# Kernel optimization log

Measured on AMD Instinct MI355X. Metric: run time of the kernel, lower is better.

## Reference

```python
import jax, jax.numpy as jnp
import numpy as np

B, L, V, D = 2048, 128, 30522, 768


def setup_inputs() -> dict:
    key = jax.random.key(0)
    k_len, k_ids, k_emb = jax.random.split(key, 3)
    # left-contiguous attention mask (HF convention), lengths in [1, L]
    lengths = jax.random.randint(k_len, (B,), 1, L + 1)
    tag_attention_mask = (jnp.arange(L)[None, :] < lengths[:, None]).astype(jnp.int32)
    tag_input_ids = jax.random.randint(k_ids, (B, L), 0, V).astype(jnp.int64)
    emb_weight = jax.random.normal(k_emb, (V, D), dtype=jnp.float32) * 0.02
    return {
        "tag_input_ids": tag_input_ids,
        "tag_attention_mask": tag_attention_mask,
        "emb_weight": emb_weight,
    }


def reference(tag_input_ids, tag_attention_mask, emb_weight):
    # embedding lookup: [B, L, D]
    tag_text_embeds = emb_weight[tag_input_ids]
    # masked mean pooling over the ragged valid prefix. Equivalent to the
    # original per-sample slice+mean loop because the mask is left-contiguous.
    m = (tag_attention_mask == 1).astype(tag_text_embeds.dtype)  # [B, L]
    summed = jnp.einsum("bld,bl->bd", tag_text_embeds, m)        # [B, D]
    counts = jnp.sum(m, axis=-1, keepdims=True)                   # [B, 1]
    return summed / counts
```

## Files before the change

### kernel.cpp

```cpp
#include <hip/hip_runtime.h>

#define BB 2048
#define LL 128
#define DD 768
#define NT 192
#define DV (DD / 4)

__global__ __launch_bounds__(NT) void masked_mean_pool_kernel(
    const int* __restrict__ ids,
    const int* __restrict__ mask,
    const float* __restrict__ emb,
    float* __restrict__ out)
{
    const int b = blockIdx.x;
    const int t = threadIdx.x;

    __shared__ int s_ids[LL];
    __shared__ int s_part[2];

    if (t < LL) {
        s_ids[t] = ids[b * LL + t];
        int m = mask[b * LL + t];
        unsigned long long bal = __ballot(m != 0);
        if ((t & 63) == 0) s_part[t >> 6] = __popcll(bal);
    }
    __syncthreads();

    const int cnt = s_part[0] + s_part[1];

    const float4* __restrict__ embv = reinterpret_cast<const float4*>(emb);

    float ax = 0.f, ay = 0.f, az = 0.f, aw = 0.f;

    int l = 0;
    for (; l + 8 <= cnt; l += 8) {
        float4 r0 = embv[s_ids[l + 0] * DV + t];
        float4 r1 = embv[s_ids[l + 1] * DV + t];
        float4 r2 = embv[s_ids[l + 2] * DV + t];
        float4 r3 = embv[s_ids[l + 3] * DV + t];
        float4 r4 = embv[s_ids[l + 4] * DV + t];
        float4 r5 = embv[s_ids[l + 5] * DV + t];
        float4 r6 = embv[s_ids[l + 6] * DV + t];
        float4 r7 = embv[s_ids[l + 7] * DV + t];
        ax += r0.x + r1.x + r2.x + r3.x + r4.x + r5.x + r6.x + r7.x;
        ay += r0.y + r1.y + r2.y + r3.y + r4.y + r5.y + r6.y + r7.y;
        az += r0.z + r1.z + r2.z + r3.z + r4.z + r5.z + r6.z + r7.z;
        aw += r0.w + r1.w + r2.w + r3.w + r4.w + r5.w + r6.w + r7.w;
    }
    for (; l < cnt; ++l) {
        float4 r = embv[s_ids[l] * DV + t];
        ax += r.x; ay += r.y; az += r.z; aw += r.w;
    }

    const float inv = 1.0f / (float)cnt;
    float4 o;
    o.x = ax * inv; o.y = ay * inv; o.z = az * inv; o.w = aw * inv;
    reinterpret_cast<float4*>(out)[b * DV + t] = o;
}

extern "C" void kernel_launch(void* const* d_in, const int* in_sizes, int n_in,
                              void* d_out, int out_size, void* d_ws, size_t ws_size,
                              hipStream_t stream) {
    const int*   ids  = (const int*)d_in[0];
    const int*   mask = (const int*)d_in[1];
    const float* emb  = (const float*)d_in[2];
    float*       out  = (float*)d_out;

    masked_mean_pool_kernel<<<BB, NT, 0, stream>>>(ids, mask, emb, out);
}
```

Baseline: 64.81 us.

## Split sequence into chunks across blocks with two-pass partial-sum reduction

Splits each batch row's sequence into four 32-token chunks, each handled by its own block that writes a partial sum to workspace. A second kernel adds the valid partials and divides by the count. The aim is to balance load across ragged lengths and raise the number of blocks for better latency hiding, at the cost of a second launch and extra workspace traffic. The old single-kernel path is kept as a fallback when the workspace is too small.

Result: slower. 83.20 us (+28.4%).

```diff
diff --git a/kernel.cpp b/kernel.cpp
--- a/kernel.cpp
+++ b/kernel.cpp
@@ -5,6 +5,93 @@
 #define DD 768
 #define NT 192
 #define DV (DD / 4)
+#define CHUNK 32
+#define CH (LL / CHUNK)
+
+__global__ __launch_bounds__(NT) void partial_sum_kernel(
+    const int* __restrict__ ids,
+    const int* __restrict__ mask,
+    const float* __restrict__ emb,
+    float* __restrict__ ws)
+{
+    const int bc = blockIdx.x;
+    const int b  = bc >> 2;
+    const int c  = bc & 3;
+    const int t  = threadIdx.x;
+
+    __shared__ int s_ids[CHUNK];
+    __shared__ int s_part[2];
+
+    if (t < LL) {
+        int m = mask[b * LL + t];
+        unsigned long long bal = __ballot(m != 0);
+        if ((t & 63) == 0) s_part[t >> 6] = __popcll(bal);
+    }
+    __syncthreads();
+    const int cnt = s_part[0] + s_part[1];
+
+    const int l0 = c * CHUNK;
+    const int n  = min(cnt, l0 + CHUNK) - l0;
+    if (n <= 0) return;
+
+    if (t < n) s_ids[t] = ids[b * LL + l0 + t];
+    __syncthreads();
+
+    const float4* __restrict__ embv = reinterpret_cast<const float4*>(emb);
+
+    float ax = 0.f, ay = 0.f, az = 0.f, aw = 0.f;
+    int l = 0;
+    for (; l + 8 <= n; l += 8) {
+        float4 r0 = embv[s_ids[l + 0] * DV + t];
+        float4 r1 = embv[s_ids[l + 1] * DV + t];
+        float4 r2 = embv[s_ids[l + 2] * DV + t];
+        float4 r3 = embv[s_ids[l + 3] * DV + t];
+        float4 r4 = embv[s_ids[l + 4] * DV + t];
+        float4 r5 = embv[s_ids[l + 5] * DV + t];
+        float4 r6 = embv[s_ids[l + 6] * DV + t];
+        float4 r7 = embv[s_ids[l + 7] * DV + t];
+        ax += r0.x + r1.x + r2.x + r3.x + r4.x + r5.x + r6.x + r7.x;
+        ay += r0.y + r1.y + r2.y + r3.y + r4.y + r5.y + r6.y + r7.y;
+        az += r0.z + r1.z + r2.z + r3.z + r4.z + r5.z + r6.z + r7.z;
+        aw += r0.w + r1.w + r2.w + r3.w + r4.w + r5.w + r6.w + r7.w;
+    }
+    for (; l < n; ++l) {
+        float4 r = embv[s_ids[l] * DV + t];
+        ax += r.x; ay += r.y; az += r.z; aw += r.w;
+    }
+
+    float4 o; o.x = ax; o.y = ay; o.z = az; o.w = aw;
+    reinterpret_cast<float4*>(ws)[bc * DV + t] = o;
+}
+
+__global__ __launch_bounds__(NT) void finalize_kernel(
+    const int* __restrict__ mask,
+    const float* __restrict__ ws,
+    float* __restrict__ out)
+{
+    const int b = blockIdx.x;
+    const int t = threadIdx.x;
+
+    __shared__ int s_part[2];
+    if (t < LL) {
+        int m = mask[b * LL + t];
+        unsigned long long bal = __ballot(m != 0);
+        if ((t & 63) == 0) s_part[t >> 6] = __popcll(bal);
+    }
+    __syncthreads();
+    const int cnt = s_part[0] + s_part[1];
+    const int nch = (cnt + CHUNK - 1) >> 5;
+
+    const float4* __restrict__ wsv = reinterpret_cast<const float4*>(ws);
+    float4 a = wsv[(b * CH + 0) * DV + t];
+    for (int c = 1; c < nch; ++c) {
+        float4 p = wsv[(b * CH + c) * DV + t];
+        a.x += p.x; a.y += p.y; a.z += p.z; a.w += p.w;
+    }
+    const float inv = 1.0f / (float)cnt;
+    a.x *= inv; a.y *= inv; a.z *= inv; a.w *= inv;
+    reinterpret_cast<float4*>(out)[b * DV + t] = a;
+}
 
 __global__ __launch_bounds__(NT) void masked_mean_pool_kernel(
     const int* __restrict__ ids,
@@ -25,13 +112,10 @@
         if ((t & 63) == 0) s_part[t >> 6] = __popcll(bal);
     }
     __syncthreads();
-
     const int cnt = s_part[0] + s_part[1];
 
     const float4* __restrict__ embv = reinterpret_cast<const float4*>(emb);
-
     float ax = 0.f, ay = 0.f, az = 0.f, aw = 0.f;
-
     int l = 0;
     for (; l + 8 <= cnt; l += 8) {
         float4 r0 = embv[s_ids[l + 0] * DV + t];
@@ -51,7 +135,6 @@
         float4 r = embv[s_ids[l] * DV + t];
         ax += r.x; ay += r.y; az += r.z; aw += r.w;
     }
-
     const float inv = 1.0f / (float)cnt;
     float4 o;
     o.x = ax * inv; o.y = ay * inv; o.z = az * inv; o.w = aw * inv;
@@ -66,5 +149,12 @@
     const float* emb  = (const float*)d_in[2];
     float*       out  = (float*)d_out;
 
-    masked_mean_pool_kernel<<<BB, NT, 0, stream>>>(ids, mask, emb, out);
+    const size_t ws_needed = (size_t)BB * CH * DD * sizeof(float);
+    if (ws_size >= ws_needed) {
+        float* ws = (float*)d_ws;
+        partial_sum_kernel<<<BB * CH, NT, 0, stream>>>(ids, mask, emb, ws);
+        finalize_kernel<<<BB, NT, 0, stream>>>(mask, ws, out);
+    } else {
+        masked_mean_pool_kernel<<<BB, NT, 0, stream>>>(ids, mask, emb, out);
+    }
 }
```
